# Optimization experiments

Hardware: AMD Instinct MI355X
Metric: run time of the kernel (lower is better)

Reference implementation:

```python
import jax, jax.numpy as jnp
import numpy as np

B, S, E, H, DK = 4, 1024, 1024, 16, 64
FF = 2048
SCALE = int(np.sqrt(DK))  # source uses int(np.sqrt(keySize)) = 8
EPS = 1e-5


def _mha(x_kv, x_q, Wq, Wk, Wv, Wo, mask):
    # Wq/Wk/Wv: [H, E, DK]; Wo: [H*DK, E]
    k = jnp.einsum('bse,hed->hbsd', x_kv, Wk)   # [H,B,S,DK]
    v = jnp.einsum('bse,hed->hbsd', x_kv, Wv)
    q = jnp.einsum('bse,hed->hbsd', x_q, Wq)
    # source does keys.reshape(B, DK, S) -- a RAW reshape, not a transpose
    kR = k.reshape(H, B, DK, S)
    scores = jnp.einsum('hbsd,hbdt->hbst', q, kR)  # [H,B,S,S]
    if mask is not None:
        scores = scores + mask  # mask added BEFORE the scale divide, as in source
    att = jax.nn.softmax(scores / SCALE, axis=-1)
    out = jnp.einsum('hbst,hbtd->hbsd', att, v)    # [H,B,S,DK]
    # source stacks heads then does a RAW reshape [H,B,S,DK] -> [B,S,DK*H]
    out = out.reshape(B, S, DK * H)
    return out @ Wo  # [B,S,E]


def _layernorm2d(x, w, b):
    # LayerNorm over last two dims (S, E) with affine params [S, E]
    m = jnp.mean(x, axis=(-2, -1), keepdims=True)
    v = jnp.var(x, axis=(-2, -1), keepdims=True)
    return (x - m) * jax.lax.rsqrt(v + EPS) * w + b


def setup_inputs() -> dict:
    key = jax.random.key(0)
    ks = jax.random.split(key, 24)
    u = lambda k, shp: jax.random.uniform(k, shp, dtype=jnp.float32)  # weights ~ U(0,1) as in source
    inp = {
        'inputRes': jax.random.normal(ks[0], (B, S, E), dtype=jnp.float32),
        'outputEncoding': jax.random.normal(ks[1], (B, S, E), dtype=jnp.float32),
        'Wq1': u(ks[2], (H, E, DK)), 'Wk1': u(ks[3], (H, E, DK)), 'Wv1': u(ks[4], (H, E, DK)),
        'Wo1': u(ks[5], (H * DK, E)),
        'Wq2': u(ks[6], (H, E, DK)), 'Wk2': u(ks[7], (H, E, DK)), 'Wv2': u(ks[8], (H, E, DK)),
        'Wo2': u(ks[9], (H * DK, E)),
        'ln1_w': jnp.ones((S, E), jnp.float32), 'ln1_b': jnp.zeros((S, E), jnp.float32),
        'ln2_w': jnp.ones((S, E), jnp.float32), 'ln2_b': jnp.zeros((S, E), jnp.float32),
        'ln3_w': jnp.ones((S, E), jnp.float32), 'ln3_b': jnp.zeros((S, E), jnp.float32),
        'W1': jax.random.normal(ks[10], (S, FF), dtype=jnp.float32) * (1.0 / np.sqrt(S)),
        'b1': jnp.zeros((FF,), jnp.float32),
        'W2': jax.random.normal(ks[11], (FF, S), dtype=jnp.float32) * (1.0 / np.sqrt(FF)),
        'b2': jnp.zeros((S,), jnp.float32),
    }
    return inp


def reference(inputRes, outputEncoding, Wq1, Wk1, Wv1, Wo1, Wq2, Wk2, Wv2, Wo2,
              ln1_w, ln1_b, ln2_w, ln2_b, ln3_w, ln3_b, W1, b1, W2, b2):
    # causal mask: row i has 0 for j<=i, -inf for j>i
    idx = jnp.arange(S)
    mask = jnp.where(idx[None, :] <= idx[:, None], 0.0, -jnp.inf).astype(jnp.float32)

    # masked self-attention + residual + LN1
    att = _mha(outputEncoding, outputEncoding, Wq1, Wk1, Wv1, Wo1, mask)
    att_norm = _layernorm2d(att + outputEncoding, ln1_w, ln1_b)

    # cross-attention (K,V from inputRes; Q from att_norm) + residual to outputEncoding + LN2
    att2 = _mha(inputRes, att_norm, Wq2, Wk2, Wv2, Wo2, None)
    att2_norm = _layernorm2d(att2 + outputEncoding, ln2_w, ln2_b)

    # FFN over the sequence dim via RAW reshape (B,S,E)->(B,E,S), as in source
    norm_res = att2_norm.reshape(B, E, S)
    fc = jax.nn.relu(norm_res @ W1 + b1) @ W2 + b2  # [B,E,S]
    fc = fc.reshape(B, S, E)

    return _layernorm2d(fc + att2_norm, ln3_w, ln3_b)
```

## Files before the change

kernel.cpp:

```cpp
#include <hip/hip_runtime.h>
#include <cstdint>
#include <cstddef>


#define DI __device__ __forceinline__
#define MFMA __builtin_amdgcn_mfma_f32_16x16x32_bf16

typedef short s8v __attribute__((ext_vector_type(8)));
typedef float f4v __attribute__((ext_vector_type(4)));
typedef unsigned u4v __attribute__((ext_vector_type(4)));

DI float bf2f(short u){
  union { unsigned int i; float f; } v;
  v.i = ((unsigned int)(unsigned short)u) << 16;
  return v.f;
}
DI short f2bf(float f){
  union { float f; unsigned int i; } v; v.f = f;
  unsigned int x = v.i;
  return (short)((x + 0x7fffu + ((x >> 16) & 1u)) >> 16);
}
DI unsigned pack2(short hi, short lo){
  return ((unsigned)(unsigned short)lo << 16) | (unsigned)(unsigned short)hi;
}
DI unsigned packf(float val){
  short hi = f2bf(val);
  return pack2(hi, f2bf(val - bf2f(hi)));
}
DI void gload16(const void* g, void* l){
  __builtin_amdgcn_global_load_lds(
      (const __attribute__((address_space(1))) unsigned*)g,
      (__attribute__((address_space(3))) unsigned*)l, 16, 0, 0);
}

struct SplitP { const float* src[2]; short* hi[2]; short* lo[2]; };

__launch_bounds__(256)
__global__ void splitall_k(SplitP sp){
  const int t = blockIdx.y;
  int i = (blockIdx.x * 256 + threadIdx.x) << 2;
  float4 v = *(const float4*)(sp.src[t] + i);
  float xs[4] = {v.x, v.y, v.z, v.w};
  short h[4], l[4];
  #pragma unroll
  for (int c = 0; c < 4; c++){
    h[c] = f2bf(xs[c]);
    l[c] = f2bf(xs[c] - bf2f(h[c]));
  }
  *(short4*)(sp.hi[t] + i) = make_short4(h[0], h[1], h[2], h[3]);
  *(short4*)(sp.lo[t] + i) = make_short4(l[0], l[1], l[2], l[3]);
}

struct TransP {
  const float* src[10];
  short* oh[10]; short* ol[10];
  int Kd[10]; int Nd[10]; int qkv[10]; int ntiles[10];
};

__launch_bounds__(256)
__global__ void transall_k(TransP tp){
  const int t = blockIdx.y;
  const int tile = blockIdx.x;
  if (tile >= tp.ntiles[t]) return;
  const int K = tp.Kd[t], N = tp.Nd[t];
  const int ncols = N >> 6;
  const int n0 = (tile % ncols) << 6, k0 = (tile / ncols) << 6;
  __shared__ float Ld[64 * 65];
  const int tid = threadIdx.x;
  const int row = tid >> 2, c16 = (tid & 3) << 4;
  const float* s = tp.src[t];
  size_t base;
  if (tp.qkv[t]) base = ((size_t)(n0 >> 6) << 16) + ((size_t)(k0 + row) << 6) + c16;
  else           base = (size_t)(k0 + row) * N + n0 + c16;
  #pragma unroll
  for (int j4 = 0; j4 < 4; j4++){
    float4 v = *(const float4*)(s + base + (j4 << 2));
    int c = row * 65 + c16 + (j4 << 2);
    Ld[c] = v.x; Ld[c + 1] = v.y; Ld[c + 2] = v.z; Ld[c + 3] = v.w;
  }
  __syncthreads();
  const int n = tid >> 2;
  s8v h0, h1, l0, l1;
  #pragma unroll
  for (int j = 0; j < 8; j++){
    float a = Ld[(c16 + j) * 65 + n];
    float b = Ld[(c16 + 8 + j) * 65 + n];
    short ha = f2bf(a), hb = f2bf(b);
    h0[j] = ha; l0[j] = f2bf(a - bf2f(ha));
    h1[j] = hb; l1[j] = f2bf(b - bf2f(hb));
  }
  size_t ob = (size_t)(n0 + n) * K + k0 + c16;
  *(s8v*)(tp.oh[t] + ob)     = h0;
  *(s8v*)(tp.oh[t] + ob + 8) = h1;
  *(s8v*)(tp.ol[t] + ob)     = l0;
  *(s8v*)(tp.ol[t] + ob + 8) = l1;
}

struct GemmP {
  const short* Ah; const short* Al; int lda;
  const short* Bh; const short* Bl; int ldb;
  int K; int N;
  const float* xres; const float* bias;
  float* outf;
  short* o1h; short* o1l;
  unsigned* p1; unsigned* p2; unsigned* p3;
};

template<int TM, int EPI, int TERMS>
__launch_bounds__(512, 2)
__global__ void gemm_k(GemmP p){
  constexpr int NG = TM / 64 + 2;
  constexpr int WM = TM >> 6;
  constexpr int NB = 128 / (8 / WM) / 16;
  __shared__ short AhL[3][TM * 32];
  __shared__ short AlL[3][TM * 32];
  __shared__ short BhL[3][128 * 32];
  __shared__ short BlL[3][128 * 32];
  const int tid = threadIdx.x;
  const int L = tid & 63, w = tid >> 6;
  const int lr = L & 15, lg = L >> 4;
  const int mo = (w & (WM - 1)) << 6;
  const int no = (w / WM) * (NB << 4);

  const int gx = gridDim.x, gy = gridDim.y;
  const int f = blockIdx.y * gx + blockIdx.x;
  const int j = f >> 3;
  const int jm = j / gx;
  const int mb = (f & 7) * (gy >> 3) + jm;
  const int nb = j - jm * gx;
  const int m0 = mb * TM, n0 = nb << 7;

  const int lrow4 = L >> 2, lcol8 = (L & 3) << 3;

  f4v acc[4][NB];
  #pragma unroll
  for (int i = 0; i < 4; i++)
    #pragma unroll
    for (int jj = 0; jj < NB; jj++)
      #pragma unroll
      for (int r = 0; r < 4; r++) acc[i][jj][r] = 0.0f;

  const int nkt = p.K >> 5;

  auto stage = [&](int tile, int slot){
    const int k0 = tile << 5;
    #pragma unroll
    for (int i = 0; i < NG; i++){
      int base_c = (i << 9) + (w << 6);
      const short* g; short* lp;
      if (base_c < TM * 4){
        int pc = base_c;
        g = p.Ah + (size_t)(m0 + (pc >> 2) + lrow4) * p.lda + k0 + lcol8;
        lp = &AhL[slot][pc << 3];
      } else if (base_c < TM * 8){
        int pc = base_c - TM * 4;
        g = p.Al + (size_t)(m0 + (pc >> 2) + lrow4) * p.lda + k0 + lcol8;
        lp = &AlL[slot][pc << 3];
      } else if (base_c < TM * 8 + 512){
        int pc = base_c - TM * 8;
        g = p.Bh + (size_t)(n0 + (pc >> 2) + lrow4) * p.ldb + k0 + lcol8;
        lp = &BhL[slot][pc << 3];
      } else {
        int pc = base_c - TM * 8 - 512;
        g = p.Bl + (size_t)(n0 + (pc >> 2) + lrow4) * p.ldb + k0 + lcol8;
        lp = &BlL[slot][pc << 3];
      }
      gload16(g, lp);
    }
  };

  stage(0, 0);
  stage(1, 1);

  for (int kt = 0; kt < nkt; kt++){
    const int cur = kt % 3;
    asm volatile("s_waitcnt vmcnt(%0)\n\ts_barrier" :: "i"(NG) : "memory");

    const int kbd = lg << 3;
    s8v a_h[4], a_l[4], b_h[NB], b_l[NB];
    #pragma unroll
    for (int mi = 0; mi < 4; mi++){
      const int row = mo + (mi << 4) + lr;
      a_h[mi] = *(const s8v*)&AhL[cur][(row << 5) + kbd];
      a_l[mi] = *(const s8v*)&AlL[cur][(row << 5) + kbd];
    }
    #pragma unroll
    for (int ni = 0; ni < NB; ni++){
      const int n = no + (ni << 4) + lr;
      b_h[ni] = *(const s8v*)&BhL[cur][(n << 5) + kbd];
      b_l[ni] = *(const s8v*)&BlL[cur][(n << 5) + kbd];
    }

    int nt = kt + 2 < nkt ? kt + 2 : nkt - 1;
    stage(nt, (kt + 2) % 3);

    #pragma unroll
    for (int ni = 0; ni < NB; ni++){
      #pragma unroll
      for (int mi = 0; mi < 4; mi++){
        acc[mi][ni] = MFMA(a_h[mi], b_h[ni], acc[mi][ni], 0, 0, 0);
        acc[mi][ni] = MFMA(a_h[mi], b_l[ni], acc[mi][ni], 0, 0, 0);
        if (TERMS == 3)
          acc[mi][ni] = MFMA(a_l[mi], b_h[ni], acc[mi][ni], 0, 0, 0);
      }
    }
  }

  #pragma unroll
  for (int mi = 0; mi < 4; mi++){
    #pragma unroll
    for (int ni = 0; ni < NB; ni++){
      #pragma unroll
      for (int r = 0; r < 4; r++){
        float val = acc[mi][ni][r];
        int m = m0 + mo + (mi << 4) + (lg << 2) + r;
        int n = n0 + no + (ni << 4) + lr;
        if (EPI == 2){
          size_t o = (size_t)m * p.N + n;
          p.outf[o] = val + p.xres[o];
        } else if (EPI == 4){
          p.outf[(size_t)m * p.N + n] = val + p.bias[n];
        } else if (EPI == 3){
          float x = val + p.bias[n];
          x = x > 0.0f ? x : 0.0f;
          size_t o = (size_t)m * p.N + n;
          short hi = f2bf(x);
          p.o1h[o] = hi;
          p.o1l[o] = f2bf(x - bf2f(hi));
        } else {
          int seg = (EPI == 0) ? 0 : (n >> 10);
          int n1 = (EPI == 0) ? n : (n & 1023);
          int kind = (EPI == 0) ? 0 : (EPI == 6 ? seg : seg + 1);
          int b = m >> 10, s = m & 1023, hh = n1 >> 6, d = n1 & 63;
          size_t hb16 = (size_t)((hh << 2) | b) << 16;
          size_t dst;
          if (kind == 0)      dst = hb16 + ((size_t)s << 6) + d;
          else if (kind == 1) dst = hb16 + ((size_t)(((s & 15) << 6) | d) << 6) + (s >> 4);
          else                dst = hb16 + ((size_t)d << 10) + s;
          unsigned* dp = (EPI == 0) ? p.p1
                       : (EPI == 6) ? (seg == 0 ? p.p1 : (seg == 1 ? p.p2 : p.p3))
                                    : (seg == 0 ? p.p1 : p.p2);
          dp[dst] = packf(val);
        }
      }
    }
  }
}

template<int CAUSAL>
__launch_bounds__(256, 2)
__global__ void flash_k(const unsigned* __restrict__ qpk,
                        const unsigned* __restrict__ kpk,
                        const unsigned* __restrict__ vpk,
                        short* __restrict__ ohi_g, short* __restrict__ olo_g){
  __shared__ short Kt[2][64*72];
  __shared__ short Vt[2][64*72];
  __shared__ unsigned Ps[2][4][16*68];
  const int tid = threadIdx.x, L = tid & 63, w = tid >> 6;
  const int lr = L & 15, lg = L >> 4;
  const int flat = blockIdx.x + (blockIdx.y << 3);
  const int hb = ((flat & 7) << 3) | ((flat >> 3) & 7);
  const int sp = flat >> 6;
  const int h = hb >> 2, b = hb & 3;
  const size_t hbo = (size_t)hb << 16;
  const float NEG_INF = -__builtin_inff();
  int qt[2]; qt[0] = sp; qt[1] = CAUSAL ? (15 - sp) : (sp + 8);

  s8v qfh[2][2], qfl[2][2];
  #pragma unroll
  for (int st = 0; st < 2; st++){
    const unsigned* qg = qpk + hbo + (size_t)((qt[st] << 6) + (w << 4) + lr) * 64 + (lg << 3);
    #pragma unroll
    for (int ks = 0; ks < 2; ks++){
      u4v p0 = *(const u4v*)(qg + (ks << 5));
      u4v p1 = *(const u4v*)(qg + (ks << 5) + 4);
      #pragma unroll
      for (int jj = 0; jj < 4; jj++){
        qfh[st][ks][jj]     = (short)(p0[jj] & 0xffffu);
        qfl[st][ks][jj]     = (short)(p0[jj] >> 16);
        qfh[st][ks][4 + jj] = (short)(p1[jj] & 0xffffu);
        qfl[st][ks][4 + jj] = (short)(p1[jj] >> 16);
      }
    }
  }

  f4v o[2][4];
  float mprev[2][4], lsum[2][4];
  #pragma unroll
  for (int st = 0; st < 2; st++){
    #pragma unroll
    for (int ni = 0; ni < 4; ni++)
      #pragma unroll
      for (int r = 0; r < 4; r++) o[st][ni][r] = 0.0f;
    #pragma unroll
    for (int r = 0; r < 4; r++){ mprev[st][r] = NEG_INF; lsum[st][r] = 0.0f; }
  }

  const int ntt = CAUSAL ? (qt[1] + 1) : 16;
  for (int ti = 0; ti < ntt; ti++){
    const int t0 = ti << 6;
    const bool actA = !(CAUSAL && ti > qt[0]);
    __syncthreads();
    {
      const int row = tid >> 2, col = (tid & 3) << 4;
      const unsigned* kg = kpk + hbo + (size_t)(t0 + row) * 64 + col;
      const unsigned* vg = vpk + hbo + ((size_t)row << 10) + t0 + col;
      unsigned kb[16], vb[16];
      #pragma unroll
      for (int j4 = 0; j4 < 4; j4++){
        *(u4v*)&kb[j4 << 2] = *(const u4v*)(kg + (j4 << 2));
        *(u4v*)&vb[j4 << 2] = *(const u4v*)(vg + (j4 << 2));
      }
      s8v kh0, kh1, kl0, kl1, vh0, vh1, vl0, vl1;
      #pragma unroll
      for (int jj = 0; jj < 8; jj++){
        kh0[jj] = (short)(kb[jj] & 0xffffu);      kl0[jj] = (short)(kb[jj] >> 16);
        kh1[jj] = (short)(kb[8 + jj] & 0xffffu);  kl1[jj] = (short)(kb[8 + jj] >> 16);
        vh0[jj] = (short)(vb[jj] & 0xffffu);      vl0[jj] = (short)(vb[jj] >> 16);
        vh1[jj] = (short)(vb[8 + jj] & 0xffffu);  vl1[jj] = (short)(vb[8 + jj] >> 16);
      }
      const int lb = row * 72 + col;
      *(s8v*)&Kt[0][lb] = kh0;  *(s8v*)&Kt[0][lb + 8] = kh1;
      *(s8v*)&Kt[1][lb] = kl0;  *(s8v*)&Kt[1][lb + 8] = kl1;
      *(s8v*)&Vt[0][lb] = vh0;  *(s8v*)&Vt[0][lb + 8] = vh1;
      *(s8v*)&Vt[1][lb] = vl0;  *(s8v*)&Vt[1][lb + 8] = vl1;
    }
    __syncthreads();

    f4v sa[2][4];
    #pragma unroll
    for (int st = 0; st < 2; st++)
      #pragma unroll
      for (int ni = 0; ni < 4; ni++)
        #pragma unroll
        for (int r = 0; r < 4; r++) sa[st][ni][r] = 0.0f;
    #pragma unroll
    for (int ks = 0; ks < 2; ks++){
      const int kb = (ks << 5) + (lg << 3);
      #pragma unroll
      for (int ni = 0; ni < 4; ni++){
        const int tl = (ni << 4) + lr;
        s8v kbh = *(const s8v*)&Kt[0][tl * 72 + kb];
        s8v kbl = *(const s8v*)&Kt[1][tl * 72 + kb];
        if (actA){
          sa[0][ni] = MFMA(qfh[0][ks], kbh, sa[0][ni], 0, 0, 0);
          sa[0][ni] = MFMA(qfh[0][ks], kbl, sa[0][ni], 0, 0, 0);
          sa[0][ni] = MFMA(qfl[0][ks], kbh, sa[0][ni], 0, 0, 0);
        }
        sa[1][ni] = MFMA(qfh[1][ks], kbh, sa[1][ni], 0, 0, 0);
        sa[1][ni] = MFMA(qfh[1][ks], kbl, sa[1][ni], 0, 0, 0);
        sa[1][ni] = MFMA(qfl[1][ks], kbh, sa[1][ni], 0, 0, 0);
      }
    }

    #pragma unroll
    for (int st = 0; st < 2; st++){
      if (st == 0 && !actA) continue;
      const int s0w = (qt[st] << 6) + (w << 4);
      const bool diag = CAUSAL && (ti == qt[st]);
      float tm[4] = {NEG_INF, NEG_INF, NEG_INF, NEG_INF};
      #pragma unroll
      for (int ni = 0; ni < 4; ni++)
        #pragma unroll
        for (int r = 0; r < 4; r++){
          float v = sa[st][ni][r] * 0.125f;
          if (diag){
            int tg = t0 + (ni << 4) + lr;
            int sg = s0w + (lg << 2) + r;
            if (tg > sg) v = NEG_INF;
          }
          sa[st][ni][r] = v;
          tm[r] = fmaxf(tm[r], v);
        }
      #pragma unroll
      for (int off = 1; off < 16; off <<= 1)
        #pragma unroll
        for (int r = 0; r < 4; r++) tm[r] = fmaxf(tm[r], __shfl_xor(tm[r], off, 16));
      float alpha[4], psum[4];
      #pragma unroll
      for (int r = 0; r < 4; r++){
        float mn = fmaxf(mprev[st][r], tm[r]);
        alpha[r] = __expf(mprev[st][r] - mn);
        mprev[st][r] = mn;
        psum[r] = 0.0f;
      }
      #pragma unroll
      for (int ni = 0; ni < 4; ni++)
        #pragma unroll
        for (int r = 0; r < 4; r++){
          float pv = __expf(sa[st][ni][r] - mprev[st][r]);
          sa[st][ni][r] = pv;
          psum[r] += pv;
        }
      #pragma unroll
      for (int off = 1; off < 16; off <<= 1)
        #pragma unroll
        for (int r = 0; r < 4; r++) psum[r] += __shfl_xor(psum[r], off, 16);
      #pragma unroll
      for (int r = 0; r < 4; r++) lsum[st][r] = lsum[st][r] * alpha[r] + psum[r];
      #pragma unroll
      for (int ni = 0; ni < 4; ni++)
        #pragma unroll
        for (int r = 0; r < 4; r++) o[st][ni][r] *= alpha[r];
      #pragma unroll
      for (int ni = 0; ni < 4; ni++)
        #pragma unroll
        for (int r = 0; r < 4; r++){
          int prow = (lg << 2) + r, pcol = (ni << 4) + lr;
          Ps[st][w][prow * 68 + pcol] = packf(sa[st][ni][r]);
        }
    }

    #pragma unroll
    for (int ks = 0; ks < 2; ks++){
      const int kb = (ks << 5) + (lg << 3);
      s8v ph[2], pl[2];
      #pragma unroll
      for (int st = 0; st < 2; st++){
        if (st == 0 && !actA) continue;
        u4v p0 = *(const u4v*)&Ps[st][w][lr * 68 + kb];
        u4v p1 = *(const u4v*)&Ps[st][w][lr * 68 + kb + 4];
        #pragma unroll
        for (int jj = 0; jj < 4; jj++){
          ph[st][jj]     = (short)(p0[jj] & 0xffffu);  pl[st][jj]     = (short)(p0[jj] >> 16);
          ph[st][4 + jj] = (short)(p1[jj] & 0xffffu);  pl[st][4 + jj] = (short)(p1[jj] >> 16);
        }
      }
      #pragma unroll
      for (int ni = 0; ni < 4; ni++){
        const int d = (ni << 4) + lr;
        s8v vbh = *(const s8v*)&Vt[0][d * 72 + kb];
        s8v vbl = *(const s8v*)&Vt[1][d * 72 + kb];
        if (actA){
          o[0][ni] = MFMA(ph[0], vbh, o[0][ni], 0, 0, 0);
          o[0][ni] = MFMA(ph[0], vbl, o[0][ni], 0, 0, 0);
          o[0][ni] = MFMA(pl[0], vbh, o[0][ni], 0, 0, 0);
        }
        o[1][ni] = MFMA(ph[1], vbh, o[1][ni], 0, 0, 0);
        o[1][ni] = MFMA(ph[1], vbl, o[1][ni], 0, 0, 0);
        o[1][ni] = MFMA(pl[1], vbh, o[1][ni], 0, 0, 0);
      }
    }
  }

  #pragma unroll
  for (int st = 0; st < 2; st++){
    const int s0w = (qt[st] << 6) + (w << 4);
    #pragma unroll
    for (int ni = 0; ni < 4; ni++){
      #pragma unroll
      for (int r = 0; r < 4; r++){
        float val = o[st][ni][r] / lsum[st][r];
        int s = s0w + (lg << 2) + r;
        int d = (ni << 4) + lr;
        int s2i = ((h & 3) << 8) | (b << 6) | (s >> 4);
        int c   = ((s & 15) << 6) | d;
        size_t dst = ((size_t)(h >> 2) << 20) + ((size_t)s2i << 10) + c;
        short hi = f2bf(val);
        ohi_g[dst] = hi;
        olo_g[dst] = f2bf(val - bf2f(hi));
      }
    }
  }
}

__launch_bounds__(256)
__global__ void ln_partial_k(const float* s1, const float* s2, float2* part){
  const int tid = threadIdx.x, L = tid & 63, w = tid >> 6;
  const int b = blockIdx.y, j = blockIdx.x;
  const size_t base = ((size_t)b << 20) + ((size_t)j << 13) + ((size_t)tid << 2);
  float sum = 0.0f, ss = 0.0f;
  #pragma unroll
  for (int i = 0; i < 8; i++){
    size_t idx = base + ((size_t)i << 10);
    float4 v = *(const float4*)(s1 + idx);
    if (s2){
      float4 u = *(const float4*)(s2 + idx);
      v.x += u.x; v.y += u.y; v.z += u.z; v.w += u.w;
    }
    sum += v.x + v.y + v.z + v.w;
    ss  += v.x*v.x + v.y*v.y + v.z*v.z + v.w*v.w;
  }
  #pragma unroll
  for (int off = 1; off < 64; off <<= 1){
    sum += __shfl_xor(sum, off, 64);
    ss  += __shfl_xor(ss,  off, 64);
  }
  __shared__ float red[4][2];
  if (L == 0){ red[w][0] = sum; red[w][1] = ss; }
  __syncthreads();
  if (tid == 0){
    float s_ = red[0][0] + red[1][0] + red[2][0] + red[3][0];
    float q_ = red[0][1] + red[1][1] + red[2][1] + red[3][1];
    part[b * 128 + j] = make_float2(s_, q_);
  }
}

__launch_bounds__(64)
__global__ void ln_final_k(const float2* part, float2* stats){
  const int b = blockIdx.x, t = threadIdx.x;
  float2 a = part[b * 128 + t], c = part[b * 128 + 64 + t];
  float sum = a.x + c.x, ss = a.y + c.y;
  #pragma unroll
  for (int off = 1; off < 64; off <<= 1){
    sum += __shfl_xor(sum, off, 64);
    ss  += __shfl_xor(ss,  off, 64);
  }
  if (t == 0){
    float mean = sum * (1.0f / 1048576.0f);
    float var  = ss  * (1.0f / 1048576.0f) - mean * mean;
    stats[b] = make_float2(mean, rsqrtf(var + 1e-5f));
  }
}

template<int MODE>
__launch_bounds__(256)
__global__ void ln_apply_k(const float* s1, const float* s2,
                           const float* wgt, const float* bias,
                           const float2* stats,
                           float* dstf, short* dsta, short* dstb){
  const int tid = threadIdx.x;
  const size_t base = ((size_t)blockIdx.x << 11) + ((size_t)tid << 2);
  #pragma unroll
  for (int i = 0; i < 2; i++){
    size_t idx = base + ((size_t)i << 10);
    int b = (int)(idx >> 20);
    float2 st = stats[b];
    float4 x = *(const float4*)(s1 + idx);
    if (s2){
      float4 u = *(const float4*)(s2 + idx);
      x.x += u.x; x.y += u.y; x.z += u.z; x.w += u.w;
    }
    unsigned wi = (unsigned)(idx & 1048575u);
    float4 wv = *(const float4*)(wgt + wi);
    float4 bv = *(const float4*)(bias + wi);
    float xv[4] = {x.x, x.y, x.z, x.w};
    float wvv[4] = {wv.x, wv.y, wv.z, wv.w};
    float bvv[4] = {bv.x, bv.y, bv.z, bv.w};
    float yv[4];
    #pragma unroll
    for (int c = 0; c < 4; c++)
      yv[c] = (xv[c] - st.x) * st.y * wvv[c] + bvv[c];
    if (MODE == 0 || MODE == 1){
      short h[4], l[4];
      #pragma unroll
      for (int c = 0; c < 4; c++){
        h[c] = f2bf(yv[c]);
        l[c] = f2bf(yv[c] - bf2f(h[c]));
      }
      *(short4*)(dsta + idx) = make_short4(h[0], h[1], h[2], h[3]);
      *(short4*)(dstb + idx) = make_short4(l[0], l[1], l[2], l[3]);
      if (MODE == 1)
        *(float4*)(dstf + idx) = make_float4(yv[0], yv[1], yv[2], yv[3]);
    } else {
      *(float4*)(dstf + idx) = make_float4(yv[0], yv[1], yv[2], yv[3]);
    }
  }
}

extern "C" void kernel_launch(void* const* d_in, const int* in_sizes, int n_in,
                              void* d_out, int out_size, void* d_ws, size_t ws_size,
                              hipStream_t stream){
  const float* IRf = (const float*)d_in[0];
  const float* OEf = (const float*)d_in[1];
  const float* Wq1f = (const float*)d_in[2];
  const float* Wk1f = (const float*)d_in[3];
  const float* Wv1f = (const float*)d_in[4];
  const float* Wo1f = (const float*)d_in[5];
  const float* Wq2f = (const float*)d_in[6];
  const float* Wk2f = (const float*)d_in[7];
  const float* Wv2f = (const float*)d_in[8];
  const float* Wo2f = (const float*)d_in[9];
  const float* ln1w = (const float*)d_in[10];
  const float* ln1b = (const float*)d_in[11];
  const float* ln2w = (const float*)d_in[12];
  const float* ln2b = (const float*)d_in[13];
  const float* ln3w = (const float*)d_in[14];
  const float* ln3b = (const float*)d_in[15];
  const float* W1f = (const float*)d_in[16];
  const float* b1f = (const float*)d_in[17];
  const float* W2f = (const float*)d_in[18];
  const float* b2f = (const float*)d_in[19];
  float* dout = (float*)d_out;

  char* ws = (char*)d_ws;
  const size_t MB = (size_t)1 << 20;
  short* OEh = (short*)(ws + 0*MB),  *OEl = (short*)(ws + 8*MB);
  short* IRh = (short*)(ws + 16*MB), *IRl = (short*)(ws + 24*MB);
  short* QKV1t_h = (short*)(ws + 32*MB), *QKV1t_l = (short*)(ws + 38*MB);
  short* Wo1t_h  = (short*)(ws + 44*MB), *Wo1t_l  = (short*)(ws + 46*MB);
  short* Q2t_h   = (short*)(ws + 48*MB), *Q2t_l   = (short*)(ws + 50*MB);
  short* KV2t_h  = (short*)(ws + 52*MB), *KV2t_l  = (short*)(ws + 56*MB);
  short* Wo2t_h  = (short*)(ws + 60*MB), *Wo2t_l  = (short*)(ws + 62*MB);
  short* W1t_h   = (short*)(ws + 64*MB), *W1t_l   = (short*)(ws + 68*MB);
  short* W2t_h   = (short*)(ws + 72*MB), *W2t_l   = (short*)(ws + 76*MB);
  unsigned* q_pk = (unsigned*)(ws + 80*MB);
  unsigned* k_pk = (unsigned*)(ws + 96*MB);
  unsigned* v_pk = (unsigned*)(ws + 112*MB);
  short* outr_h = (short*)(ws + 128*MB), *outr_l = (short*)(ws + 136*MB);
  float* resid = (float*)(ws + 144*MB);
  short* attn_h = (short*)(ws + 160*MB), *attn_l = (short*)(ws + 168*MB);
  float* att2n_f = (float*)(ws + 176*MB);
  short* hid_h = (short*)(ws + 80*MB);
  short* hid_l = (short*)(ws + 96*MB);
  float* fc    = (float*)(ws + 112*MB);
  short* a2n_h = (short*)(ws + 160*MB);
  short* a2n_l = (short*)(ws + 168*MB);
  float2* part  = (float2*)(ws + 192*MB);
  float2* stats = (float2*)(ws + 192*MB + 65536);

  dim3 blk(256), blkg(512);

  SplitP sp;
  sp.src[0] = OEf; sp.hi[0] = OEh; sp.lo[0] = OEl;
  sp.src[1] = IRf; sp.hi[1] = IRh; sp.lo[1] = IRl;
  splitall_k<<<dim3(4096, 2), blk, 0, stream>>>(sp);

  TransP tp;
  const float* tsrc[10] = {Wq1f, Wk1f, Wv1f, Wo1f, Wq2f, Wk2f, Wv2f, Wo2f, W1f, W2f};
  short* toh[10] = {QKV1t_h, QKV1t_h + (1<<20), QKV1t_h + (2<<20), Wo1t_h,
                    Q2t_h, KV2t_h, KV2t_h + (1<<20), Wo2t_h, W1t_h, W2t_h};
  short* tol[10] = {QKV1t_l, QKV1t_l + (1<<20), QKV1t_l + (2<<20), Wo1t_l,
                    Q2t_l, KV2t_l, KV2t_l + (1<<20), Wo2t_l, W1t_l, W2t_l};
  int tK[10]   = {1024,1024,1024,1024,1024,1024,1024,1024,1024,2048};
  int tN[10]   = {1024,1024,1024,1024,1024,1024,1024,1024,2048,1024};
  int tq[10]   = {1,1,1,0,1,1,1,0,0,0};
  int tt[10]   = {256,256,256,256,256,256,256,256,512,512};
  for (int i = 0; i < 10; i++){
    tp.src[i] = tsrc[i]; tp.oh[i] = toh[i]; tp.ol[i] = tol[i];
    tp.Kd[i] = tK[i]; tp.Nd[i] = tN[i]; tp.qkv[i] = tq[i]; tp.ntiles[i] = tt[i];
  }
  transall_k<<<dim3(512, 10), blk, 0, stream>>>(tp);

  GemmP p{};

  p = {OEh, OEl, 1024, QKV1t_h, QKV1t_l, 1024, 1024, 3072, nullptr, nullptr,
       nullptr, nullptr, nullptr, q_pk, k_pk, v_pk};
  gemm_k<256,6,3><<<dim3(24, 16), blkg, 0, stream>>>(p);
  flash_k<1><<<dim3(8, 64), blk, 0, stream>>>(q_pk, k_pk, v_pk, outr_h, outr_l);
  p = {outr_h, outr_l, 1024, Wo1t_h, Wo1t_l, 1024, 1024, 1024, OEf, nullptr,
       resid, nullptr, nullptr, nullptr, nullptr, nullptr};
  gemm_k<128,2,3><<<dim3(8, 32), blkg, 0, stream>>>(p);
  ln_partial_k<<<dim3(128, 4), blk, 0, stream>>>(resid, nullptr, part);
  ln_final_k<<<dim3(4), dim3(64), 0, stream>>>(part, stats);
  ln_apply_k<0><<<dim3(2048), blk, 0, stream>>>(resid, nullptr, ln1w, ln1b, stats, nullptr, attn_h, attn_l);

  p = {attn_h, attn_l, 1024, Q2t_h, Q2t_l, 1024, 1024, 1024, nullptr, nullptr,
       nullptr, nullptr, nullptr, q_pk, nullptr, nullptr};
  gemm_k<128,0,3><<<dim3(8, 32), blkg, 0, stream>>>(p);
  p = {IRh, IRl, 1024, KV2t_h, KV2t_l, 1024, 1024, 2048, nullptr, nullptr,
       nullptr, nullptr, nullptr, k_pk, v_pk, nullptr};
  gemm_k<256,7,3><<<dim3(16, 16), blkg, 0, stream>>>(p);
  flash_k<0><<<dim3(8, 64), blk, 0, stream>>>(q_pk, k_pk, v_pk, outr_h, outr_l);
  p = {outr_h, outr_l, 1024, Wo2t_h, Wo2t_l, 1024, 1024, 1024, OEf, nullptr,
       resid, nullptr, nullptr, nullptr, nullptr, nullptr};
  gemm_k<128,2,3><<<dim3(8, 32), blkg, 0, stream>>>(p);
  ln_partial_k<<<dim3(128, 4), blk, 0, stream>>>(resid, nullptr, part);
  ln_final_k<<<dim3(4), dim3(64), 0, stream>>>(part, stats);
  ln_apply_k<1><<<dim3(2048), blk, 0, stream>>>(resid, nullptr, ln2w, ln2b, stats, att2n_f, a2n_h, a2n_l);

  p = {a2n_h, a2n_l, 1024, W1t_h, W1t_l, 1024, 1024, 2048, nullptr, b1f,
       nullptr, hid_h, hid_l, nullptr, nullptr, nullptr};
  gemm_k<256,3,2><<<dim3(16, 16), blkg, 0, stream>>>(p);
  p = {hid_h, hid_l, 2048, W2t_h, W2t_l, 2048, 2048, 1024, nullptr, b2f,
       fc, nullptr, nullptr, nullptr, nullptr, nullptr};
  gemm_k<128,4,2><<<dim3(8, 32), blkg, 0, stream>>>(p);
  ln_partial_k<<<dim3(128, 4), blk, 0, stream>>>(fc, att2n_f, part);
  ln_final_k<<<dim3(4), dim3(64), 0, stream>>>(part, stats);
  ln_apply_k<2><<<dim3(2048), blk, 0, stream>>>(fc, att2n_f, ln3w, ln3b, stats, dout, nullptr, nullptr);
}
```

Before: 741.1 us.

## Swizzle LDS tiles, skip unused A-low plane, interleave loads with MFMA phases

Restructures the split-bf16 GEMM main loop into phases. Each phase loads one operand plane from LDS, issues part of the next tile's global-to-LDS copies, then runs its MFMA batch under raised wave priority, with barriers between phases. It adds an XOR swizzle on the k-column within each LDS row to cut bank conflicts. For 2-term GEMMs it no longer allocates or stages the A-low plane, which saves LDS and global traffic. The extra barriers per k-tile could add sync overhead, and the swizzle has to match exactly between writes and reads.

```diff
diff --git a/kernel.cpp b/kernel.cpp
--- a/kernel.cpp
+++ b/kernel.cpp
@@ -109,11 +109,11 @@
 template<int TM, int EPI, int TERMS>
 __launch_bounds__(512, 2)
 __global__ void gemm_k(GemmP p){
-  constexpr int NG = TM / 64 + 2;
+  constexpr int NG = (TERMS == 3) ? (TM / 64 + 2) : (TM / 128 + 2);
   constexpr int WM = TM >> 6;
   constexpr int NB = 128 / (8 / WM) / 16;
   __shared__ short AhL[3][TM * 32];
-  __shared__ short AlL[3][TM * 32];
+  __shared__ short AlL[3][(TERMS == 3) ? TM * 32 : 8];
   __shared__ short BhL[3][128 * 32];
   __shared__ short BlL[3][128 * 32];
   const int tid = threadIdx.x;
@@ -130,7 +130,19 @@
   const int nb = j - jm * gx;
   const int m0 = mb * TM, n0 = nb << 7;
 
-  const int lrow4 = L >> 2, lcol8 = (L & 3) << 3;
+  const int lrow4 = L >> 2, lq = L & 3;
+
+  int aoff[4], boff[NB];
+  #pragma unroll
+  for (int mi = 0; mi < 4; mi++){
+    int r = mo + (mi << 4) + lr;
+    aoff[mi] = (r << 5) + ((lg ^ ((r >> 1) & 3)) << 3);
+  }
+  #pragma unroll
+  for (int ni = 0; ni < NB; ni++){
+    int n = no + (ni << 4) + lr;
+    boff[ni] = (n << 5) + ((lg ^ ((n >> 1) & 3)) << 3);
+  }
 
   f4v acc[4][NB];
   #pragma unroll
@@ -142,67 +154,82 @@
 
   const int nkt = p.K >> 5;
 
-  auto stage = [&](int tile, int slot){
+  auto stage1 = [&](int tile, int slot, int i){
     const int k0 = tile << 5;
-    #pragma unroll
-    for (int i = 0; i < NG; i++){
-      int base_c = (i << 9) + (w << 6);
-      const short* g; short* lp;
-      if (base_c < TM * 4){
-        int pc = base_c;
-        g = p.Ah + (size_t)(m0 + (pc >> 2) + lrow4) * p.lda + k0 + lcol8;
-        lp = &AhL[slot][pc << 3];
-      } else if (base_c < TM * 8){
-        int pc = base_c - TM * 4;
-        g = p.Al + (size_t)(m0 + (pc >> 2) + lrow4) * p.lda + k0 + lcol8;
-        lp = &AlL[slot][pc << 3];
-      } else if (base_c < TM * 8 + 512){
-        int pc = base_c - TM * 8;
-        g = p.Bh + (size_t)(n0 + (pc >> 2) + lrow4) * p.ldb + k0 + lcol8;
-        lp = &BhL[slot][pc << 3];
-      } else {
-        int pc = base_c - TM * 8 - 512;
-        g = p.Bl + (size_t)(n0 + (pc >> 2) + lrow4) * p.ldb + k0 + lcol8;
-        lp = &BlL[slot][pc << 3];
-      }
-      gload16(g, lp);
-    }
+    int base_c = (i << 9) + (w << 6);
+    const short* plane; short* lds; int row0; int ld; int pc;
+    if (base_c < TM * 4){
+      pc = base_c; plane = p.Ah; lds = &AhL[slot][0]; row0 = m0; ld = p.lda;
+    } else if (TERMS == 3 && base_c < TM * 8){
+      pc = base_c - TM * 4; plane = p.Al; lds = &AlL[slot][0]; row0 = m0; ld = p.lda;
+    } else {
+      int pc2 = base_c - (TERMS == 3 ? TM * 8 : TM * 4);
+      if (pc2 < 512){ pc = pc2; plane = p.Bh; lds = &BhL[slot][0]; }
+      else          { pc = pc2 - 512; plane = p.Bl; lds = &BlL[slot][0]; }
+      row0 = n0; ld = p.ldb;
+    }
+    int rl = (pc >> 2) + lrow4;
+    int sc = (lq ^ ((rl >> 1) & 3)) << 3;
+    gload16(plane + (size_t)(row0 + rl) * ld + k0 + sc, lds + (pc << 3));
   };
 
-  stage(0, 0);
-  stage(1, 1);
+  #pragma unroll
+  for (int i = 0; i < NG; i++) stage1(0, 0, i);
+  #pragma unroll
+  for (int i = 0; i < NG; i++) stage1(1, 1, i);
 
   for (int kt = 0; kt < nkt; kt++){
     const int cur = kt % 3;
+    const int nt = kt + 2 < nkt ? kt + 2 : nkt - 1;
+    const int nslot = (kt + 2) % 3;
     asm volatile("s_waitcnt vmcnt(%0)\n\ts_barrier" :: "i"(NG) : "memory");
 
-    const int kbd = lg << 3;
-    s8v a_h[4], a_l[4], b_h[NB], b_l[NB];
-    #pragma unroll
-    for (int mi = 0; mi < 4; mi++){
-      const int row = mo + (mi << 4) + lr;
-      a_h[mi] = *(const s8v*)&AhL[cur][(row << 5) + kbd];
-      a_l[mi] = *(const s8v*)&AlL[cur][(row << 5) + kbd];
-    }
-    #pragma unroll
-    for (int ni = 0; ni < NB; ni++){
-      const int n = no + (ni << 4) + lr;
-      b_h[ni] = *(const s8v*)&BhL[cur][(n << 5) + kbd];
-      b_l[ni] = *(const s8v*)&BlL[cur][(n << 5) + kbd];
-    }
-
-    int nt = kt + 2 < nkt ? kt + 2 : nkt - 1;
-    stage(nt, (kt + 2) % 3);
-
-    #pragma unroll
-    for (int ni = 0; ni < NB; ni++){
-      #pragma unroll
-      for (int mi = 0; mi < 4; mi++){
+    s8v a_h[4], b_h[NB];
+    #pragma unroll
+    for (int mi = 0; mi < 4; mi++) a_h[mi] = *(const s8v*)&AhL[cur][aoff[mi]];
+    #pragma unroll
+    for (int ni = 0; ni < NB; ni++) b_h[ni] = *(const s8v*)&BhL[cur][boff[ni]];
+    stage1(nt, nslot, 0);
+    stage1(nt, nslot, 1);
+    __builtin_amdgcn_s_barrier();
+    __builtin_amdgcn_s_setprio(1);
+    #pragma unroll
+    for (int ni = 0; ni < NB; ni++)
+      #pragma unroll
+      for (int mi = 0; mi < 4; mi++)
         acc[mi][ni] = MFMA(a_h[mi], b_h[ni], acc[mi][ni], 0, 0, 0);
+    __builtin_amdgcn_s_setprio(0);
+    __builtin_amdgcn_s_barrier();
+
+    s8v b_l[NB];
+    #pragma unroll
+    for (int ni = 0; ni < NB; ni++) b_l[ni] = *(const s8v*)&BlL[cur][boff[ni]];
+    if (NG > 2) stage1(nt, nslot, 2);
+    if (NG > 3) stage1(nt, nslot, 3);
+    __builtin_amdgcn_s_barrier();
+    __builtin_amdgcn_s_setprio(1);
+    #pragma unroll
+    for (int ni = 0; ni < NB; ni++)
+      #pragma unroll
+      for (int mi = 0; mi < 4; mi++)
         acc[mi][ni] = MFMA(a_h[mi], b_l[ni], acc[mi][ni], 0, 0, 0);
-        if (TERMS == 3)
+    __builtin_amdgcn_s_setprio(0);
+
+    if (TERMS == 3){
+      __builtin_amdgcn_s_barrier();
+      s8v a_l[4];
+      #pragma unroll
+      for (int mi = 0; mi < 4; mi++) a_l[mi] = *(const s8v*)&AlL[cur][aoff[mi]];
+      if (NG > 4) stage1(nt, nslot, 4);
+      if (NG > 5) stage1(nt, nslot, 5);
+      __builtin_amdgcn_s_barrier();
+      __builtin_amdgcn_s_setprio(1);
+      #pragma unroll
+      for (int ni = 0; ni < NB; ni++)
+        #pragma unroll
+        for (int mi = 0; mi < 4; mi++)
           acc[mi][ni] = MFMA(a_l[mi], b_h[ni], acc[mi][ni], 0, 0, 0);
-      }
+      __builtin_amdgcn_s_setprio(0);
     }
   }
 
```

Result: no change. 738.6 us (-0.3%).

## Swizzle GEMM LDS layout and skip loading unused A-low plane for two-term GEMMs

Applied to the files above, without the earlier changes.

Applies an XOR swizzle to the k-chunk position within each LDS row, on both the global-to-LDS load path and the fragment reads, to reduce LDS bank conflicts. For the two-term split-bf16 GEMM variant, the A-low plane is no longer staged or read, which cuts global loads and LDS footprint. The loop's wait count now follows the reduced number of load groups per stage.

```diff
diff --git a/kernel.cpp b/kernel.cpp
--- a/kernel.cpp
+++ b/kernel.cpp
@@ -109,11 +109,13 @@
 template<int TM, int EPI, int TERMS>
 __launch_bounds__(512, 2)
 __global__ void gemm_k(GemmP p){
-  constexpr int NG = TM / 64 + 2;
+  constexpr int AGR = TM * 4;
+  constexpr int NGRAN = (TERMS == 3 ? 2 * AGR : AGR) + 1024;
+  constexpr int NG = NGRAN >> 9;
   constexpr int WM = TM >> 6;
   constexpr int NB = 128 / (8 / WM) / 16;
   __shared__ short AhL[3][TM * 32];
-  __shared__ short AlL[3][TM * 32];
+  __shared__ short AlL[3][(TERMS == 3) ? TM * 32 : 8];
   __shared__ short BhL[3][128 * 32];
   __shared__ short BlL[3][128 * 32];
   const int tid = threadIdx.x;
@@ -130,7 +132,19 @@
   const int nb = j - jm * gx;
   const int m0 = mb * TM, n0 = nb << 7;
 
-  const int lrow4 = L >> 2, lcol8 = (L & 3) << 3;
+  const int lrow4 = L >> 2, lq = L & 3;
+
+  int aoff[4], boff[NB];
+  #pragma unroll
+  for (int mi = 0; mi < 4; mi++){
+    int r = mo + (mi << 4) + lr;
+    aoff[mi] = (r << 5) + ((lg ^ ((r >> 1) & 3)) << 3);
+  }
+  #pragma unroll
+  for (int ni = 0; ni < NB; ni++){
+    int n = no + (ni << 4) + lr;
+    boff[ni] = (n << 5) + ((lg ^ ((n >> 1) & 3)) << 3);
+  }
 
   f4v acc[4][NB];
   #pragma unroll
@@ -147,25 +161,20 @@
     #pragma unroll
     for (int i = 0; i < NG; i++){
       int base_c = (i << 9) + (w << 6);
-      const short* g; short* lp;
-      if (base_c < TM * 4){
-        int pc = base_c;
-        g = p.Ah + (size_t)(m0 + (pc >> 2) + lrow4) * p.lda + k0 + lcol8;
-        lp = &AhL[slot][pc << 3];
-      } else if (base_c < TM * 8){
-        int pc = base_c - TM * 4;
-        g = p.Al + (size_t)(m0 + (pc >> 2) + lrow4) * p.lda + k0 + lcol8;
-        lp = &AlL[slot][pc << 3];
-      } else if (base_c < TM * 8 + 512){
-        int pc = base_c - TM * 8;
-        g = p.Bh + (size_t)(n0 + (pc >> 2) + lrow4) * p.ldb + k0 + lcol8;
-        lp = &BhL[slot][pc << 3];
+      const short* plane; short* lds; int row0; int ld; int pc;
+      if (base_c < AGR){
+        pc = base_c; plane = p.Ah; lds = &AhL[slot][0]; row0 = m0; ld = p.lda;
+      } else if (TERMS == 3 && base_c < 2 * AGR){
+        pc = base_c - AGR; plane = p.Al; lds = &AlL[slot][0]; row0 = m0; ld = p.lda;
       } else {
-        int pc = base_c - TM * 8 - 512;
-        g = p.Bl + (size_t)(n0 + (pc >> 2) + lrow4) * p.ldb + k0 + lcol8;
-        lp = &BlL[slot][pc << 3];
-      }
-      gload16(g, lp);
+        int pc2 = base_c - (TERMS == 3 ? 2 * AGR : AGR);
+        if (pc2 < 512){ pc = pc2; plane = p.Bh; lds = &BhL[slot][0]; }
+        else          { pc = pc2 - 512; plane = p.Bl; lds = &BlL[slot][0]; }
+        row0 = n0; ld = p.ldb;
+      }
+      int rl = (pc >> 2) + lrow4;
+      int sc = (lq ^ ((rl >> 1) & 3)) << 3;
+      gload16(plane + (size_t)(row0 + rl) * ld + k0 + sc, lds + (pc << 3));
     }
   };
 
@@ -176,19 +185,16 @@
     const int cur = kt % 3;
     asm volatile("s_waitcnt vmcnt(%0)\n\ts_barrier" :: "i"(NG) : "memory");
 
-    const int kbd = lg << 3;
     s8v a_h[4], a_l[4], b_h[NB], b_l[NB];
     #pragma unroll
     for (int mi = 0; mi < 4; mi++){
-      const int row = mo + (mi << 4) + lr;
-      a_h[mi] = *(const s8v*)&AhL[cur][(row << 5) + kbd];
-      a_l[mi] = *(const s8v*)&AlL[cur][(row << 5) + kbd];
+      a_h[mi] = *(const s8v*)&AhL[cur][aoff[mi]];
+      if (TERMS == 3) a_l[mi] = *(const s8v*)&AlL[cur][aoff[mi]];
     }
     #pragma unroll
     for (int ni = 0; ni < NB; ni++){
-      const int n = no + (ni << 4) + lr;
-      b_h[ni] = *(const s8v*)&BhL[cur][(n << 5) + kbd];
-      b_l[ni] = *(const s8v*)&BlL[cur][(n << 5) + kbd];
+      b_h[ni] = *(const s8v*)&BhL[cur][boff[ni]];
+      b_l[ni] = *(const s8v*)&BlL[cur][boff[ni]];
     }
 
     int nt = kt + 2 < nkt ? kt + 2 : nkt - 1;
```

Measured after the change: 690.7 us. -6.8%, faster.
